# Optimization experiments

Measured on AMD Instinct MI355X. Metric: run time of the kernel, lower is better.

Reference implementation:

```python
import jax, jax.numpy as jnp
import numpy as np

N_HEAD = 32
N_KV_HEAD = 8
ROPE_THETA = 500000.0


def rotate_half(x):
    d = x.shape[-1] // 2
    return jnp.concatenate((-x[..., d:], x[..., :d]), axis=-1)


def setup_inputs() -> dict:
    key = jax.random.key(0)
    ks = jax.random.split(key, 5)
    C = 2048
    B, T = 2, 2048
    s = 1.0 / np.sqrt(C)
    return {
        "x": jax.random.normal(ks[0], (B, T, C), dtype=jnp.float32),
        "Wq": jax.random.normal(ks[1], (C, C), dtype=jnp.float32) * s,
        "Wk": jax.random.normal(ks[2], (C, 512), dtype=jnp.float32) * s,
        "Wv": jax.random.normal(ks[3], (C, 512), dtype=jnp.float32) * s,
        "Wo": jax.random.normal(ks[4], (C, C), dtype=jnp.float32) * s,
    }


def reference(x, Wq, Wk, Wv, Wo):
    B, T, C = x.shape
    H, KV = N_HEAD, N_KV_HEAD
    D = C // H
    n_rep = H // KV

    q = (x @ Wq).reshape(B, T, H, D).transpose(0, 2, 1, 3)   # [B,H,T,D]
    k = (x @ Wk).reshape(B, T, KV, D).transpose(0, 2, 1, 3)  # [B,KV,T,D]
    v = (x @ Wv).reshape(B, T, KV, D).transpose(0, 2, 1, 3)  # [B,KV,T,D]

    # RoPE: cos/sin of shape [1,1,T,D], broadcast over batch and heads
    inv_freq = 1.0 / (ROPE_THETA ** (jnp.arange(0, D, 2, dtype=jnp.float32) / D))
    freqs = jnp.arange(T, dtype=jnp.float32)[:, None] * inv_freq[None, :]  # [T,D/2]
    emb = jnp.concatenate((freqs, freqs), axis=-1)  # [T,D]
    cos = jnp.cos(emb)[None, None].astype(x.dtype)
    sin = jnp.sin(emb)[None, None].astype(x.dtype)

    q = q * cos + rotate_half(q) * sin
    k = k * cos + rotate_half(k) * sin

    # repeat_kv (GQA expansion): [B,KV,T,D] -> [B,H,T,D]
    k = jnp.repeat(k, n_rep, axis=1)
    v = jnp.repeat(v, n_rep, axis=1)

    scale = 1.0 / jnp.sqrt(jnp.asarray(D, dtype=x.dtype))
    scores = jnp.einsum("bhqd,bhkd->bhqk", q, k) * scale  # [B,H,T,T]
    causal = jnp.tril(jnp.ones((T, T), dtype=bool))
    scores = jnp.where(causal[None, None], scores, jnp.finfo(scores.dtype).min)
    attn = jax.nn.softmax(scores, axis=-1)
    y = jnp.einsum("bhqk,bhkd->bhqd", attn, v)  # [B,H,T,D]
    y = y.transpose(0, 2, 1, 3).reshape(B, T, C)
    return y @ Wo
```

## Files before the change

### kernel.cpp

```cpp
#include <hip/hip_runtime.h>

using u16 = unsigned short;
using u32 = unsigned int;

typedef __attribute__((ext_vector_type(8))) __bf16 bf16x8;
typedef __attribute__((ext_vector_type(4))) float f32x4;
typedef __attribute__((ext_vector_type(16))) float f32x16;

#define DEVI __device__ __forceinline__

DEVI float bf2f(u16 u) {
  union { u32 i; float f; } v; v.i = ((u32)u) << 16; return v.f;
}
DEVI u16 f2bf(float f) {
  union { float f; u32 u; } v; v.f = f;
  u32 u = v.u;
  u32 r = (u + 0x7fffu + ((u >> 16) & 1u)) >> 16;
  return (u16)r;
}
DEVI u32 pkbf(float a, float b) {
  union { __bf16 h[2]; u32 u; } t;
  t.h[0] = (__bf16)a; t.h[1] = (__bf16)b;
  return t.u;
}

DEVI void gload16(const u16* g, u16* l) {
  __builtin_amdgcn_global_load_lds(
      (const __attribute__((address_space(1))) void*)g,
      (__attribute__((address_space(3))) void*)l, 16, 0, 0);
}

__global__ __launch_bounds__(256) void cvt_bf16_f32(const float* __restrict__ in,
                                                    u16* __restrict__ out, int n8) {
  int i = blockIdx.x * 256 + threadIdx.x;
  if (i >= n8) return;
  const float4* fin = (const float4*)in;
  float4 a = fin[i * 2], b = fin[i * 2 + 1];
  u16 o[8] = {f2bf(a.x), f2bf(a.y), f2bf(a.z), f2bf(a.w),
              f2bf(b.x), f2bf(b.y), f2bf(b.z), f2bf(b.w)};
  ((uint4*)out)[i] = *(const uint4*)o;
}

DEVI void tcvt64_body(const float* in, u16* out, int R, int Cc, int c0, int r0, int t,
                      u16 (*tile)[72]) {
  {
    int row = t >> 2, part = t & 3;
    const float* src = in + (size_t)(r0 + row) * Cc + c0 + part * 16;
    float4 f0 = ((const float4*)src)[0];
    float4 f1 = ((const float4*)src)[1];
    float4 f2 = ((const float4*)src)[2];
    float4 f3 = ((const float4*)src)[3];
    u16 v[16] = {f2bf(f0.x), f2bf(f0.y), f2bf(f0.z), f2bf(f0.w),
                 f2bf(f1.x), f2bf(f1.y), f2bf(f1.z), f2bf(f1.w),
                 f2bf(f2.x), f2bf(f2.y), f2bf(f2.z), f2bf(f2.w),
                 f2bf(f3.x), f2bf(f3.y), f2bf(f3.z), f2bf(f3.w)};
    *(uint4*)&tile[row][part * 16]     = ((const uint4*)v)[0];
    *(uint4*)&tile[row][part * 16 + 8] = ((const uint4*)v)[1];
  }
  __syncthreads();
  {
    int c = t & 63, rq = t >> 6;
    u16 v[16];
#pragma unroll
    for (int i = 0; i < 16; i++) v[i] = tile[rq * 16 + i][c];
    u16* dst = out + (size_t)(c0 + c) * R + r0 + rq * 16;
    ((uint4*)dst)[0] = ((const uint4*)v)[0];
    ((uint4*)dst)[1] = ((const uint4*)v)[1];
  }
}

__global__ __launch_bounds__(256) void transpose_cvt64(const float* __restrict__ in,
                                                       u16* __restrict__ out,
                                                       int R, int Cc) {
  __shared__ u16 tile[64][72];
  tcvt64_body(in, out, R, Cc, blockIdx.x * 64, blockIdx.y * 64, threadIdx.x, tile);
}

__global__ __launch_bounds__(256) void transpose_wqkv(const float* __restrict__ Wq,
                                                      const float* __restrict__ Wk,
                                                      const float* __restrict__ Wv,
                                                      u16* __restrict__ out) {
  __shared__ u16 tile[64][72];
  int bx = blockIdx.x;
  const float* in;
  u16* dst;
  int Cc, c0;
  if (bx < 32)      { in = Wq; dst = out;                        Cc = 2048; c0 = bx * 64; }
  else if (bx < 40) { in = Wk; dst = out + (size_t)2048 * 2048;  Cc = 512;  c0 = (bx - 32) * 64; }
  else              { in = Wv; dst = out + (size_t)2560 * 2048;  Cc = 512;  c0 = (bx - 40) * 64; }
  tcvt64_body(in, dst, 2048, Cc, c0, blockIdx.y * 64, threadIdx.x, tile);
}

__global__ __launch_bounds__(256) void transpose_sl64(const u16* __restrict__ in, int ldin,
                                                      u16* __restrict__ out,
                                                      int R, int Cc) {
  __shared__ u16 tile[64][72];
  int c0 = blockIdx.x * 64, r0 = blockIdx.y * 64;
  int t = threadIdx.x;
  {
    int row = t >> 2, part = t & 3;
    const u16* src = in + (size_t)(r0 + row) * ldin + c0 + part * 16;
    uint4 a = ((const uint4*)src)[0];
    uint4 b = ((const uint4*)src)[1];
    *(uint4*)&tile[row][part * 16]     = a;
    *(uint4*)&tile[row][part * 16 + 8] = b;
  }
  __syncthreads();
  {
    int c = t & 63, rq = t >> 6;
    u16 v[16];
#pragma unroll
    for (int i = 0; i < 16; i++) v[i] = tile[rq * 16 + i][c];
    u16* dst = out + (size_t)(c0 + c) * R + r0 + rq * 16;
    ((uint4*)dst)[0] = ((const uint4*)v)[0];
    ((uint4*)dst)[1] = ((const uint4*)v)[1];
  }
}

DEVI void rope_body(u16* X, int h4shift, float scale, int idx) {
  int hq   = idx & ((1 << h4shift) - 1);
  int row  = idx >> h4shift;
  int head = hq >> 2;
  int d0   = (hq & 3) * 8;
  int tpos = row & 2047;
  size_t base = (size_t)row * 3072 + head * 64 + d0;
  uint4 lo = *(const uint4*)(X + base);
  uint4 hi = *(const uint4*)(X + base + 32);
  const u16* lp = (const u16*)&lo;
  const u16* hp = (const u16*)&hi;
  float ang = (float)tpos * exp2f(-(float)d0 * 0.59161152f);
  u16 o0[8], o1[8];
#pragma unroll
  for (int i = 0; i < 8; i++) {
    float s, c;
    __sincosf(ang, &s, &c);
    s *= scale; c *= scale;
    float x0 = bf2f(lp[i]);
    float x1 = bf2f(hp[i]);
    o0[i] = f2bf(x0 * c - x1 * s);
    o1[i] = f2bf(x1 * c + x0 * s);
    ang *= 0.6636011f;
  }
  *(uint4*)(X + base)      = *(const uint4*)o0;
  *(uint4*)(X + base + 32) = *(const uint4*)o1;
}

__global__ __launch_bounds__(256) void rope_fused(u16* __restrict__ QKV) {
  const int NQ = 4096 * 128;
  int idx = blockIdx.x * 256 + threadIdx.x;
  if (idx < NQ) rope_body(QKV, 7, 0.18033688f, idx);
  else          rope_body(QKV + 2048, 5, 1.0f, idx - NQ);
}

DEVI void cstore(u16* C, size_t idx, float v)   { C[idx] = f2bf(v); }
DEVI void cstore(float* C, size_t idx, float v) { C[idx] = v; }

template <typename TO>
__global__ __launch_bounds__(256) void gemm128(const u16* __restrict__ A,
                                               const u16* __restrict__ Bt,
                                               TO* __restrict__ C,
                                               int M, int N, int K) {
  __shared__ u16 As[2 * 128 * 32];
  __shared__ u16 Bs[2 * 128 * 32];
  int tid = threadIdx.x, wid = tid >> 6, lane = tid & 63;
  int quad = lane >> 4, l15 = lane & 15;
  int m0 = blockIdx.y * 128, n0 = blockIdx.x * 128;
  int wm = (wid >> 1) * 64, wn = (wid & 1) * 64;

  int r0s = wid * 16 + (lane >> 2);
  int r1s = 64 + wid * 16 + (lane >> 2);
  int cblk = lane & 3;
  int cs0 = (cblk ^ ((r0s >> 1) & 3)) * 8;
  int cs1 = (cblk ^ ((r1s >> 1) & 3)) * 8;
  u16* lA0 = As + wid * 512 + lane * 8;
  u16* lA1 = As + (4 + wid) * 512 + lane * 8;
  u16* lB0 = Bs + wid * 512 + lane * 8;
  u16* lB1 = Bs + (4 + wid) * 512 + lane * 8;
  const u16* gA0 = A + (size_t)(m0 + r0s) * K + cs0;
  const u16* gA1 = A + (size_t)(m0 + r1s) * K + cs1;
  const u16* gB0 = Bt + (size_t)(n0 + r0s) * K + cs0;
  const u16* gB1 = Bt + (size_t)(n0 + r1s) * K + cs1;

  f32x4 acc[4][4];
  for (int i = 0; i < 4; i++)
    for (int j = 0; j < 4; j++) acc[i][j] = f32x4{0.f, 0.f, 0.f, 0.f};

  gload16(gA0, lA0);
  gload16(gA1, lA1);
  gload16(gB0, lB0);
  gload16(gB1, lB1);
  __builtin_amdgcn_s_waitcnt(0x0F70);
  __syncthreads();

  int cur = 0;
  for (int k0 = 0; k0 < K; k0 += 32) {
    int nb = cur ^ 1;
    if (k0 + 32 < K) {
      gload16(gA0 + k0 + 32, lA0 + nb * 4096);
      gload16(gA1 + k0 + 32, lA1 + nb * 4096);
      gload16(gB0 + k0 + 32, lB0 + nb * 4096);
      gload16(gB1 + k0 + 32, lB1 + nb * 4096);
    }
    const u16* Ab = As + cur * 4096;
    const u16* Bb = Bs + cur * 4096;
    bf16x8 af[4], bf_[4];
    for (int mi = 0; mi < 4; mi++) {
      int row = wm + mi * 16 + l15;
      af[mi] = *(const bf16x8*)(Ab + row * 32 + ((quad ^ ((row >> 1) & 3)) * 8));
    }
    for (int ni = 0; ni < 4; ni++) {
      int row = wn + ni * 16 + l15;
      bf_[ni] = *(const bf16x8*)(Bb + row * 32 + ((quad ^ ((row >> 1) & 3)) * 8));
    }
    for (int mi = 0; mi < 4; mi++)
      for (int ni = 0; ni < 4; ni++)
        acc[mi][ni] = __builtin_amdgcn_mfma_f32_16x16x32_bf16(af[mi], bf_[ni], acc[mi][ni], 0, 0, 0);
    __builtin_amdgcn_s_waitcnt(0x0F70);
    __syncthreads();
    cur = nb;
  }
  for (int mi = 0; mi < 4; mi++)
    for (int ni = 0; ni < 4; ni++)
      for (int r = 0; r < 4; r++) {
        int row = m0 + wm + mi * 16 + quad * 4 + r;
        int col = n0 + wn + ni * 16 + l15;
        cstore(C, (size_t)row * N + col, acc[mi][ni][r]);
      }
}

__global__ __launch_bounds__(256) void attn64(const u16* __restrict__ QKV,
                                              const u16* __restrict__ Vt,
                                              u16* __restrict__ Y) {
  __shared__ u16 Ks[2 * 64 * 64];
  __shared__ u16 Vst[2 * 64 * 64];

  int tid = threadIdx.x, wid = tid >> 6, lane = tid & 63;
  int l31 = lane & 31, hi = lane >> 5;
  int bh = blockIdx.y, b = bh >> 5, h = bh & 31, kvh = h >> 2;
  int j = 15 - blockIdx.x;

  int kr  = wid * 8 + (lane >> 3);
  int kgn = lane & 7;
  const u16* gK0 = QKV + (size_t)(b * 2048 + kr) * 3072 + 2048 + kvh * 64
                 + ((kgn ^ (kr & 7)) * 8);
  u16* lK0 = Ks + wid * 512 + lane * 8;

  int vr = tid >> 3, vg = tid & 7;
  const u16* gV0 = Vt + (size_t)(kvh * 64 + vr) * 4096 + b * 2048 + vg * 8;
  u16* lV0 = Vst + vr * 64 + ((vg ^ (vr & 7)) * 8);

  f32x16 fzero;
#pragma unroll
  for (int i = 0; i < 16; i++) fzero[i] = 0.f;

  int q0w = j * 128 + wid * 32;
  int qg  = q0w + l31;

  bf16x8 qf[4];
  {
    const u16* qp = QKV + (size_t)(b * 2048 + qg) * 3072 + h * 64 + hi * 8;
#pragma unroll
    for (int dh = 0; dh < 4; dh++) qf[dh] = *(const bf16x8*)(qp + dh * 16);
  }

  f32x16 o0, o1;
#pragma unroll
  for (int i = 0; i < 16; i++) { o0[i] = 0.f; o1[i] = 0.f; }
  float zsum = 0.f;

  int nkt = 2 * (j + 1);

  {
    uint4 va = *(const uint4*)(gV0);
    uint4 vb = *(const uint4*)(gV0 + 32 * 4096);
    gload16(gK0, lK0);
    gload16(gK0 + 32 * 3072, lK0 + 2048);
    __builtin_amdgcn_s_waitcnt(0x0F70);
    *(uint4*)(lV0)        = va;
    *(uint4*)(lV0 + 2048) = vb;
  }
  __syncthreads();

  int cur = 0;
  for (int kt = 0; kt < nkt; kt++) {
    int kbase = kt * 64;
    int nxt = cur ^ 1;
    bool more = (kt + 1 < nkt);
    uint4 va, vb;
    if (more) {
      size_t ko = (size_t)(kbase + 64);
      va = *(const uint4*)(gV0 + ko);
      vb = *(const uint4*)(gV0 + 32 * 4096 + ko);
      gload16(gK0 + ko * 3072, lK0 + nxt * 4096);
      gload16(gK0 + ko * 3072 + 32 * 3072, lK0 + nxt * 4096 + 2048);
    }

    const u16* Kb = Ks + cur * 4096;
    const u16* Vb = Vst + cur * 4096;
#pragma unroll
    for (int sub = 0; sub < 2; sub++) {
      int kb = kbase + sub * 32;
      if (kb > q0w) break;

      bf16x8 kf0 = *(const bf16x8*)(Kb + (sub * 32 + l31) * 64 + ((hi ^ (l31 & 7)) * 8));
      f32x16 s = __builtin_amdgcn_mfma_f32_32x32x16_bf16(kf0, qf[0], fzero, 0, 0, 0);
#pragma unroll
      for (int dh = 1; dh < 4; dh++) {
        int g = (dh * 2 + hi) ^ (l31 & 7);
        bf16x8 kf = *(const bf16x8*)(Kb + (sub * 32 + l31) * 64 + g * 8);
        s = __builtin_amdgcn_mfma_f32_32x32x16_bf16(kf, qf[dh], s, 0, 0, 0);
      }

      float pb[16];
      if (kb < q0w) {
#pragma unroll
        for (int r = 0; r < 16; r++) {
          float pv = exp2f(s[r]);
          zsum += pv;
          pb[r] = pv;
        }
      } else {
#pragma unroll
        for (int r = 0; r < 16; r++) {
          int key = kb + (r & 3) + 8 * (r >> 2) + 4 * hi;
          float pv = (key <= qg) ? exp2f(s[r]) : 0.f;
          zsum += pv;
          pb[r] = pv;
        }
      }

#pragma unroll
      for (int kk = 0; kk < 2; kk++) {
        const float* pp = pb + kk * 8;
        u32 a01 = pkbf(pp[0], pp[1]);
        u32 a23 = pkbf(pp[2], pp[3]);
        u32 a45 = pkbf(pp[4], pp[5]);
        u32 a67 = pkbf(pp[6], pp[7]);
        asm volatile("v_permlane32_swap_b32 %0, %1" : "+v"(a01), "+v"(a45));
        asm volatile("v_permlane32_swap_b32 %0, %1" : "+v"(a23), "+v"(a67));
        union { u32 w[4]; bf16x8 v; } pf;
        pf.w[0] = a01; pf.w[1] = a23; pf.w[2] = a45; pf.w[3] = a67;
        int kgr = sub * 4 + kk * 2 + hi;
        const u16* vp = Vb + l31 * 64 + ((kgr ^ (l31 & 7)) * 8);
        bf16x8 v0 = *(const bf16x8*)(vp);
        bf16x8 v1 = *(const bf16x8*)(vp + 2048);
        o0 = __builtin_amdgcn_mfma_f32_32x32x16_bf16(pf.v, v0, o0, 0, 0, 0);
        o1 = __builtin_amdgcn_mfma_f32_32x32x16_bf16(pf.v, v1, o1, 0, 0, 0);
      }
    }

    if (more) {
      __builtin_amdgcn_s_waitcnt(0x0F70);
      *(uint4*)(lV0 + nxt * 4096)        = va;
      *(uint4*)(lV0 + nxt * 4096 + 2048) = vb;
    }
    __syncthreads();
    cur = nxt;
  }

  float zf = zsum + __shfl_xor(zsum, 32);

#pragma unroll
  for (int r = 0; r < 16; r++) {
    int qr = (r & 3) + 8 * (r >> 2) + 4 * hi;
    float zr = __shfl(zf, qr, 64);
    float inv = 1.f / zr;
    size_t row = (size_t)(b * 2048 + q0w + qr);
    Y[row * 2048 + h * 64 + l31]      = f2bf(o0[r] * inv);
    Y[row * 2048 + h * 64 + 32 + l31] = f2bf(o1[r] * inv);
  }
}

extern "C" void kernel_launch(void* const* d_in, const int* in_sizes, int n_in,
                              void* d_out, int out_size, void* d_ws, size_t ws_size,
                              hipStream_t stream) {
  const float* x  = (const float*)d_in[0];
  const float* Wq = (const float*)d_in[1];
  const float* Wk = (const float*)d_in[2];
  const float* Wv = (const float*)d_in[3];
  const float* Wo = (const float*)d_in[4];
  float* outp = (float*)d_out;

  u16* xb    = (u16*)d_ws;
  u16* WqkvT = xb + 8388608;
  u16* QKV   = WqkvT + 6291456;
  u16* Vt    = QKV + 12582912;
  u16* Yb    = xb;
  u16* WoT   = WqkvT;

  cvt_bf16_f32<<<4096, 256, 0, stream>>>(x, xb, 1048576);

  transpose_wqkv<<<dim3(48, 32), 256, 0, stream>>>(Wq, Wk, Wv, WqkvT);

  gemm128<u16><<<dim3(24, 32), 256, 0, stream>>>(xb, WqkvT, QKV, 4096, 3072, 2048);

  rope_fused<<<2560, 256, 0, stream>>>(QKV);

  transpose_sl64<<<dim3(8, 64), 256, 0, stream>>>(QKV + 2560, 3072, Vt, 4096, 512);

  attn64<<<dim3(16, 64), 256, 0, stream>>>(QKV, Vt, Yb);

  transpose_cvt64<<<dim3(32, 32), 256, 0, stream>>>(Wo, WoT, 2048, 2048);
  gemm128<float><<<dim3(16, 32), 256, 0, stream>>>(Yb, WoT, outp, 4096, 2048, 2048);
}
```

Baseline: 364.6 us.

## Fuse RoPE into QKV GEMM epilogue, swizzle GEMM blocks, pair causal attention tiles

Removes the standalone RoPE kernel and applies the rotation and the softmax scale inside the QKV GEMM epilogue, saving one read-modify-write pass over Q and K. It also remaps GEMM workgroup IDs with a grouped swizzle to improve L2 reuse. The attention grid is halved, and each block processes query tile p and tile 15-p in sequence, so causal work per block is balanced. Risks include the swizzle assuming a grid size divisible by 8, and fewer attention blocks reducing parallelism.

Measured after the change: 310.5 us. 14.8% less time.

```diff
diff --git a/kernel.cpp b/kernel.cpp
--- a/kernel.cpp
+++ b/kernel.cpp
@@ -117,45 +117,10 @@
   }
 }
 
-DEVI void rope_body(u16* X, int h4shift, float scale, int idx) {
-  int hq   = idx & ((1 << h4shift) - 1);
-  int row  = idx >> h4shift;
-  int head = hq >> 2;
-  int d0   = (hq & 3) * 8;
-  int tpos = row & 2047;
-  size_t base = (size_t)row * 3072 + head * 64 + d0;
-  uint4 lo = *(const uint4*)(X + base);
-  uint4 hi = *(const uint4*)(X + base + 32);
-  const u16* lp = (const u16*)&lo;
-  const u16* hp = (const u16*)&hi;
-  float ang = (float)tpos * exp2f(-(float)d0 * 0.59161152f);
-  u16 o0[8], o1[8];
-#pragma unroll
-  for (int i = 0; i < 8; i++) {
-    float s, c;
-    __sincosf(ang, &s, &c);
-    s *= scale; c *= scale;
-    float x0 = bf2f(lp[i]);
-    float x1 = bf2f(hp[i]);
-    o0[i] = f2bf(x0 * c - x1 * s);
-    o1[i] = f2bf(x1 * c + x0 * s);
-    ang *= 0.6636011f;
-  }
-  *(uint4*)(X + base)      = *(const uint4*)o0;
-  *(uint4*)(X + base + 32) = *(const uint4*)o1;
-}
-
-__global__ __launch_bounds__(256) void rope_fused(u16* __restrict__ QKV) {
-  const int NQ = 4096 * 128;
-  int idx = blockIdx.x * 256 + threadIdx.x;
-  if (idx < NQ) rope_body(QKV, 7, 0.18033688f, idx);
-  else          rope_body(QKV + 2048, 5, 1.0f, idx - NQ);
-}
-
 DEVI void cstore(u16* C, size_t idx, float v)   { C[idx] = f2bf(v); }
 DEVI void cstore(float* C, size_t idx, float v) { C[idx] = v; }
 
-template <typename TO>
+template <typename TO, bool ROPE>
 __global__ __launch_bounds__(256) void gemm128(const u16* __restrict__ A,
                                                const u16* __restrict__ Bt,
                                                TO* __restrict__ C,
@@ -164,7 +129,12 @@
   __shared__ u16 Bs[2 * 128 * 32];
   int tid = threadIdx.x, wid = tid >> 6, lane = tid & 63;
   int quad = lane >> 4, l15 = lane & 15;
-  int m0 = blockIdx.y * 128, n0 = blockIdx.x * 128;
+
+  int nwg = gridDim.x * gridDim.y;
+  int bid = blockIdx.y * gridDim.x + blockIdx.x;
+  int swz = (bid & 7) * (nwg >> 3) + (bid >> 3);
+  int bx = swz % gridDim.x, by = swz / gridDim.x;
+  int m0 = by * 128, n0 = bx * 128;
   int wm = (wid >> 1) * 64, wn = (wid & 1) * 64;
 
   int r0s = wid * 16 + (lane >> 2);
@@ -219,6 +189,29 @@
     __syncthreads();
     cur = nb;
   }
+
+  if (ROPE) {
+#pragma unroll
+    for (int ni = 0; ni < 2; ni++) {
+      int nc = n0 + wn + ni * 16;
+      if (nc < 2560) {
+        float scale = (nc < 2048) ? 0.18033688f : 1.0f;
+        float inv = exp2f(-(float)(ni * 16 + l15) * 0.59161152f);
+#pragma unroll
+        for (int mi = 0; mi < 4; mi++)
+#pragma unroll
+          for (int r = 0; r < 4; r++) {
+            int t = (m0 + wm + mi * 16 + quad * 4 + r) & 2047;
+            float sn, cs;
+            __sincosf((float)t * inv, &sn, &cs);
+            float xl = acc[mi][ni][r], xh = acc[mi][ni + 2][r];
+            acc[mi][ni][r]     = (xl * cs - xh * sn) * scale;
+            acc[mi][ni + 2][r] = (xh * cs + xl * sn) * scale;
+          }
+      }
+    }
+  }
+
   for (int mi = 0; mi < 4; mi++)
     for (int ni = 0; ni < 4; ni++)
       for (int r = 0; r < 4; r++) {
@@ -237,7 +230,7 @@
   int tid = threadIdx.x, wid = tid >> 6, lane = tid & 63;
   int l31 = lane & 31, hi = lane >> 5;
   int bh = blockIdx.y, b = bh >> 5, h = bh & 31, kvh = h >> 2;
-  int j = 15 - blockIdx.x;
+  int p = blockIdx.x;
 
   int kr  = wid * 8 + (lane >> 3);
   int kgn = lane & 7;
@@ -249,125 +242,125 @@
   const u16* gV0 = Vt + (size_t)(kvh * 64 + vr) * 4096 + b * 2048 + vg * 8;
   u16* lV0 = Vst + vr * 64 + ((vg ^ (vr & 7)) * 8);
 
-  f32x16 fzero;
-#pragma unroll
-  for (int i = 0; i < 16; i++) fzero[i] = 0.f;
-
-  int q0w = j * 128 + wid * 32;
-  int qg  = q0w + l31;
-
-  bf16x8 qf[4];
-  {
-    const u16* qp = QKV + (size_t)(b * 2048 + qg) * 3072 + h * 64 + hi * 8;
-#pragma unroll
-    for (int dh = 0; dh < 4; dh++) qf[dh] = *(const bf16x8*)(qp + dh * 16);
-  }
-
-  f32x16 o0, o1;
-#pragma unroll
-  for (int i = 0; i < 16; i++) { o0[i] = 0.f; o1[i] = 0.f; }
-  float zsum = 0.f;
-
-  int nkt = 2 * (j + 1);
-
-  {
-    uint4 va = *(const uint4*)(gV0);
-    uint4 vb = *(const uint4*)(gV0 + 32 * 4096);
-    gload16(gK0, lK0);
-    gload16(gK0 + 32 * 3072, lK0 + 2048);
-    __builtin_amdgcn_s_waitcnt(0x0F70);
-    *(uint4*)(lV0)        = va;
-    *(uint4*)(lV0 + 2048) = vb;
-  }
-  __syncthreads();
-
-  int cur = 0;
-  for (int kt = 0; kt < nkt; kt++) {
-    int kbase = kt * 64;
-    int nxt = cur ^ 1;
-    bool more = (kt + 1 < nkt);
-    uint4 va, vb;
-    if (more) {
-      size_t ko = (size_t)(kbase + 64);
-      va = *(const uint4*)(gV0 + ko);
-      vb = *(const uint4*)(gV0 + 32 * 4096 + ko);
-      gload16(gK0 + ko * 3072, lK0 + nxt * 4096);
-      gload16(gK0 + ko * 3072 + 32 * 3072, lK0 + nxt * 4096 + 2048);
-    }
-
-    const u16* Kb = Ks + cur * 4096;
-    const u16* Vb = Vst + cur * 4096;
-#pragma unroll
-    for (int sub = 0; sub < 2; sub++) {
-      int kb = kbase + sub * 32;
-      if (kb > q0w) break;
-
-      bf16x8 kf0 = *(const bf16x8*)(Kb + (sub * 32 + l31) * 64 + ((hi ^ (l31 & 7)) * 8));
-      f32x16 s = __builtin_amdgcn_mfma_f32_32x32x16_bf16(kf0, qf[0], fzero, 0, 0, 0);
-#pragma unroll
-      for (int dh = 1; dh < 4; dh++) {
-        int g = (dh * 2 + hi) ^ (l31 & 7);
-        bf16x8 kf = *(const bf16x8*)(Kb + (sub * 32 + l31) * 64 + g * 8);
-        s = __builtin_amdgcn_mfma_f32_32x32x16_bf16(kf, qf[dh], s, 0, 0, 0);
-      }
-
-      float pb[16];
-      if (kb < q0w) {
-#pragma unroll
-        for (int r = 0; r < 16; r++) {
-          float pv = exp2f(s[r]);
-          zsum += pv;
-          pb[r] = pv;
+  for (int pass = 0; pass < 2; pass++) {
+    int j   = pass ? (15 - p) : p;
+    int q0w = j * 128 + wid * 32;
+    int qg  = q0w + l31;
+
+    bf16x8 qf[4];
+    {
+      const u16* qp = QKV + (size_t)(b * 2048 + qg) * 3072 + h * 64 + hi * 8;
+#pragma unroll
+      for (int dh = 0; dh < 4; dh++) qf[dh] = *(const bf16x8*)(qp + dh * 16);
+    }
+
+    f32x16 o0, o1;
+#pragma unroll
+    for (int i = 0; i < 16; i++) { o0[i] = 0.f; o1[i] = 0.f; }
+    float zsum = 0.f;
+
+    int nkt = 2 * (j + 1);
+
+    {
+      uint4 va = *(const uint4*)(gV0);
+      uint4 vb = *(const uint4*)(gV0 + 32 * 4096);
+      gload16(gK0, lK0);
+      gload16(gK0 + 32 * 3072, lK0 + 2048);
+      __builtin_amdgcn_s_waitcnt(0x0F70);
+      *(uint4*)(lV0)        = va;
+      *(uint4*)(lV0 + 2048) = vb;
+    }
+    __syncthreads();
+
+    int cur = 0;
+    for (int kt = 0; kt < nkt; kt++) {
+      int kbase = kt * 64;
+      int nxt = cur ^ 1;
+      bool more = (kt + 1 < nkt);
+      uint4 va, vb;
+      if (more) {
+        size_t ko = (size_t)(kbase + 64);
+        va = *(const uint4*)(gV0 + ko);
+        vb = *(const uint4*)(gV0 + 32 * 4096 + ko);
+        gload16(gK0 + ko * 3072, lK0 + nxt * 4096);
+        gload16(gK0 + ko * 3072 + 32 * 3072, lK0 + nxt * 4096 + 2048);
+      }
+
+      const u16* Kb = Ks + cur * 4096;
+      const u16* Vb = Vst + cur * 4096;
+#pragma unroll
+      for (int sub = 0; sub < 2; sub++) {
+        int kb = kbase + sub * 32;
+        if (kb > q0w) break;
+
+        f32x16 s;
+#pragma unroll
+        for (int i = 0; i < 16; i++) s[i] = 0.f;
+#pragma unroll
+        for (int dh = 0; dh < 4; dh++) {
+          int g = (dh * 2 + hi) ^ (l31 & 7);
+          bf16x8 kf = *(const bf16x8*)(Kb + (sub * 32 + l31) * 64 + g * 8);
+          s = __builtin_amdgcn_mfma_f32_32x32x16_bf16(kf, qf[dh], s, 0, 0, 0);
         }
-      } else {
-#pragma unroll
-        for (int r = 0; r < 16; r++) {
-          int key = kb + (r & 3) + 8 * (r >> 2) + 4 * hi;
-          float pv = (key <= qg) ? exp2f(s[r]) : 0.f;
-          zsum += pv;
-          pb[r] = pv;
+
+        float pb[16];
+        if (kb < q0w) {
+#pragma unroll
+          for (int r = 0; r < 16; r++) {
+            float pv = exp2f(s[r]);
+            zsum += pv;
+            pb[r] = pv;
+          }
+        } else {
+#pragma unroll
+          for (int r = 0; r < 16; r++) {
+            int key = kb + (r & 3) + 8 * (r >> 2) + 4 * hi;
+            float pv = (key <= qg) ? exp2f(s[r]) : 0.f;
+            zsum += pv;
+            pb[r] = pv;
+          }
         }
-      }
-
-#pragma unroll
-      for (int kk = 0; kk < 2; kk++) {
-        const float* pp = pb + kk * 8;
-        u32 a01 = pkbf(pp[0], pp[1]);
-        u32 a23 = pkbf(pp[2], pp[3]);
-        u32 a45 = pkbf(pp[4], pp[5]);
-        u32 a67 = pkbf(pp[6], pp[7]);
-        asm volatile("v_permlane32_swap_b32 %0, %1" : "+v"(a01), "+v"(a45));
-        asm volatile("v_permlane32_swap_b32 %0, %1" : "+v"(a23), "+v"(a67));
-        union { u32 w[4]; bf16x8 v; } pf;
-        pf.w[0] = a01; pf.w[1] = a23; pf.w[2] = a45; pf.w[3] = a67;
-        int kgr = sub * 4 + kk * 2 + hi;
-        const u16* vp = Vb + l31 * 64 + ((kgr ^ (l31 & 7)) * 8);
-        bf16x8 v0 = *(const bf16x8*)(vp);
-        bf16x8 v1 = *(const bf16x8*)(vp + 2048);
-        o0 = __builtin_amdgcn_mfma_f32_32x32x16_bf16(pf.v, v0, o0, 0, 0, 0);
-        o1 = __builtin_amdgcn_mfma_f32_32x32x16_bf16(pf.v, v1, o1, 0, 0, 0);
-      }
-    }
-
-    if (more) {
-      __builtin_amdgcn_s_waitcnt(0x0F70);
-      *(uint4*)(lV0 + nxt * 4096)        = va;
-      *(uint4*)(lV0 + nxt * 4096 + 2048) = vb;
-    }
-    __syncthreads();
-    cur = nxt;
-  }
-
-  float zf = zsum + __shfl_xor(zsum, 32);
-
-#pragma unroll
-  for (int r = 0; r < 16; r++) {
-    int qr = (r & 3) + 8 * (r >> 2) + 4 * hi;
-    float zr = __shfl(zf, qr, 64);
-    float inv = 1.f / zr;
-    size_t row = (size_t)(b * 2048 + q0w + qr);
-    Y[row * 2048 + h * 64 + l31]      = f2bf(o0[r] * inv);
-    Y[row * 2048 + h * 64 + 32 + l31] = f2bf(o1[r] * inv);
+
+#pragma unroll
+        for (int kk = 0; kk < 2; kk++) {
+          const float* pp = pb + kk * 8;
+          u32 a01 = pkbf(pp[0], pp[1]);
+          u32 a23 = pkbf(pp[2], pp[3]);
+          u32 a45 = pkbf(pp[4], pp[5]);
+          u32 a67 = pkbf(pp[6], pp[7]);
+          asm volatile("v_permlane32_swap_b32 %0, %1" : "+v"(a01), "+v"(a45));
+          asm volatile("v_permlane32_swap_b32 %0, %1" : "+v"(a23), "+v"(a67));
+          union { u32 w[4]; bf16x8 v; } pf;
+          pf.w[0] = a01; pf.w[1] = a23; pf.w[2] = a45; pf.w[3] = a67;
+          int kgr = sub * 4 + kk * 2 + hi;
+          const u16* vp = Vb + l31 * 64 + ((kgr ^ (l31 & 7)) * 8);
+          bf16x8 v0 = *(const bf16x8*)(vp);
+          bf16x8 v1 = *(const bf16x8*)(vp + 2048);
+          o0 = __builtin_amdgcn_mfma_f32_32x32x16_bf16(pf.v, v0, o0, 0, 0, 0);
+          o1 = __builtin_amdgcn_mfma_f32_32x32x16_bf16(pf.v, v1, o1, 0, 0, 0);
+        }
+      }
+
+      if (more) {
+        __builtin_amdgcn_s_waitcnt(0x0F70);
+        *(uint4*)(lV0 + nxt * 4096)        = va;
+        *(uint4*)(lV0 + nxt * 4096 + 2048) = vb;
+      }
+      __syncthreads();
+      cur = nxt;
+    }
+
+    float zf = zsum + __shfl_xor(zsum, 32);
+
+#pragma unroll
+    for (int r = 0; r < 16; r++) {
+      int qr = (r & 3) + 8 * (r >> 2) + 4 * hi;
+      float zr = __shfl(zf, qr, 64);
+      float inv = 1.f / zr;
+      size_t row = (size_t)(b * 2048 + q0w + qr);
+      Y[row * 2048 + h * 64 + l31]      = f2bf(o0[r] * inv);
+      Y[row * 2048 + h * 64 + 32 + l31] = f2bf(o1[r] * inv);
+    }
   }
 }
 
@@ -392,14 +385,12 @@
 
   transpose_wqkv<<<dim3(48, 32), 256, 0, stream>>>(Wq, Wk, Wv, WqkvT);
 
-  gemm128<u16><<<dim3(24, 32), 256, 0, stream>>>(xb, WqkvT, QKV, 4096, 3072, 2048);
-
-  rope_fused<<<2560, 256, 0, stream>>>(QKV);
+  gemm128<u16, true><<<dim3(24, 32), 256, 0, stream>>>(xb, WqkvT, QKV, 4096, 3072, 2048);
 
   transpose_sl64<<<dim3(8, 64), 256, 0, stream>>>(QKV + 2560, 3072, Vt, 4096, 512);
 
-  attn64<<<dim3(16, 64), 256, 0, stream>>>(QKV, Vt, Yb);
+  attn64<<<dim3(8, 64), 256, 0, stream>>>(QKV, Vt, Yb);
 
   transpose_cvt64<<<dim3(32, 32), 256, 0, stream>>>(Wo, WoT, 2048, 2048);
-  gemm128<float><<<dim3(16, 32), 256, 0, stream>>>(Yb, WoT, outp, 4096, 2048, 2048);
-}
+  gemm128<float, false><<<dim3(16, 32), 256, 0, stream>>>(Yb, WoT, outp, 4096, 2048, 2048);
+}
```
